# Performance work log

Measured on AMD Instinct MI355X. Metric: run time of the kernel, lower is better.

The kernel has to match this reference:

```python
import jax, jax.numpy as jnp
import numpy as np
from jax import lax

NUM_SUPERNODES = 1024
KNN_K = 16
MIN_GRIPPER = 16
MIN_MASK = 8
GRIP_START = 0
GRIP_RADIUS = 0.1
NEG_INF = -jnp.inf


def _take(a, idx):
    return jnp.take_along_axis(a, idx, axis=1)


def _scatter_or(idx, keep, Bf, N):
    # OR `keep` into a fresh [Bf,N] bool mask at positions idx (mirrors torch scatter_)
    b = jnp.arange(Bf)[:, None]
    return jnp.zeros((Bf, N), dtype=bool).at[b, idx].max(keep)


def _cdist(a, b):
    # a [B,M,3], b [B,N,3] -> [B,M,N] euclidean
    d2 = (jnp.sum(a * a, -1)[:, :, None] + jnp.sum(b * b, -1)[:, None, :]
          - 2.0 * jnp.einsum('bmd,bnd->bmn', a, b))
    return jnp.sqrt(jnp.maximum(d2, 0.0))


def _sample_supernodes(xyz, valid, state, mask_id, extra_scores, global_scores):
    Bf, N, _ = xyz.shape
    M = NUM_SUPERNODES
    valid = valid.astype(bool)
    row_has_valid = valid.any(axis=1)
    first_valid = jnp.argmax(valid, axis=1).astype(jnp.int32)  # [Bf]

    # ---- gripper quota: nearest points to gripper xyz (within radius if any) ----
    k_grip = min(MIN_GRIPPER, M)
    gxyz = state[:, GRIP_START:GRIP_START + 3]
    gdist = jnp.linalg.norm(xyz - gxyz[:, None, :], axis=-1)  # [Bf,N]
    in_radius = gdist <= GRIP_RADIUS
    has_radius = (valid & in_radius).any(axis=1, keepdims=True)
    eligible = valid & (in_radius | ~has_radius)
    dist_rank = jnp.where(eligible, gdist, jnp.inf)
    neg_vals, grip_idx = lax.top_k(-dist_rank, k_grip)
    grip_vals = -neg_vals
    grip_keep = jnp.isfinite(grip_vals) & row_has_valid[:, None]
    head_idx = jnp.where(grip_keep, grip_idx, first_valid[:, None])
    head_bucket = jnp.where(grip_keep, 1, -1)
    selected = _scatter_or(grip_idx, grip_keep, Bf, N)

    remaining = M - k_grip
    # ---- mask-instance quota: one point per mask id (dedup via sort) ----
    mask_cand = valid & ~selected
    sentinel = jnp.iinfo(mask_id.dtype).max
    mask_key = jnp.where(mask_cand, mask_id, sentinel)
    sort_idx = jnp.argsort(mask_key, axis=1)
    sorted_valid = _take(mask_cand, sort_idx)
    sorted_mask = _take(mask_id, sort_idx)
    first_for_id = jnp.concatenate(
        [sorted_valid[:, :1],
         sorted_valid[:, 1:] & (sorted_mask[:, 1:] != sorted_mask[:, :-1])], axis=1)
    pos = jnp.arange(N, dtype=jnp.float32)[None, :]
    mask_scores = jnp.where(first_for_id, -pos, NEG_INF)
    mask_vals, mask_pos = lax.top_k(mask_scores, remaining)
    mask_idx = _take(sort_idx, mask_pos)
    mask_keep = jnp.isfinite(mask_vals) & row_has_valid[:, None]
    selected_after_mask = selected | _scatter_or(mask_idx, mask_keep, Bf, N)

    # ---- extra random mask supernodes to guarantee min_mask quota ----
    k_extra = min(MIN_MASK, remaining)
    es = jnp.where(valid & ~selected_after_mask, extra_scores, NEG_INF)
    extra_vals, extra_idx = lax.top_k(es, k_extra)
    extra_keep = jnp.isfinite(extra_vals) & row_has_valid[:, None]
    use_extra = ~mask_keep[:, :k_extra] & extra_keep
    mask_idx = mask_idx.at[:, :k_extra].set(
        jnp.where(use_extra, extra_idx, mask_idx[:, :k_extra]))
    mask_keep = mask_keep.at[:, :k_extra].set(mask_keep[:, :k_extra] | use_extra)

    # ---- global random fill ----
    selected_for_global = selected | _scatter_or(mask_idx, mask_keep, Bf, N)
    gs = jnp.where(valid & ~selected_for_global, global_scores, NEG_INF)
    gvals, gidx = lax.top_k(gs, remaining)
    gkeep = jnp.isfinite(gvals) & row_has_valid[:, None]
    fill_idx = jnp.where(mask_keep, mask_idx,
                         jnp.where(gkeep, gidx, first_valid[:, None]))
    fill_bucket = jnp.where(mask_keep, 2, jnp.where(gkeep, 0, -1))

    out_idx = jnp.concatenate([head_idx, fill_idx], axis=1)
    out_bucket = jnp.concatenate([head_bucket, fill_bucket], axis=1)
    out_valid = _take(valid, out_idx) & row_has_valid[:, None]
    out_bucket = jnp.where(out_valid, out_bucket, -1)
    return out_idx, out_valid, out_bucket


def setup_inputs() -> dict:
    key = jax.random.key(0)
    ks = jax.random.split(key, 6)
    Bf, N, C = 8, 16384, 64
    return {
        'x': jax.random.normal(ks[0], (Bf, N, C), dtype=jnp.float32),
        'xyz': jax.random.normal(ks[1], (Bf, N, 3), dtype=jnp.float32),
        'valid': jnp.ones((Bf, N), dtype=bool),
        'state': jax.random.normal(ks[2], (Bf, 8), dtype=jnp.float32),
        'mask_id': jax.random.randint(ks[3], (Bf, N), 0, 32, dtype=jnp.int32),
        'extra_scores': jax.random.uniform(ks[4], (Bf, N), dtype=jnp.float32),
        'global_scores': jax.random.uniform(ks[5], (Bf, N), dtype=jnp.float32),
    }


def reference(x, xyz, valid, state, mask_id, extra_scores, global_scores):
    Bf, N, C = x.shape
    out_idx, out_valid, out_bucket = _sample_supernodes(
        xyz, valid, state, mask_id, extra_scores, global_scores)
    # gather_points
    supernode_xyz = _take(xyz, out_idx[:, :, None].repeat(3, axis=2))  # [Bf,M,3]
    # build_knn_neighbors: masked cdist + topk smallest
    dist = _cdist(supernode_xyz.astype(jnp.float32), xyz.astype(jnp.float32))
    dist = jnp.where(valid.astype(bool)[:, None, :], dist, jnp.inf)
    neg_vals, neighbor_idx = lax.top_k(-dist, KNN_K)
    neighbor_mask = jnp.isfinite(-neg_vals)  # [Bf,M,K]
    # gather_neighbors
    b = jnp.arange(Bf)[:, None, None]
    neighbor_feats = x[b, neighbor_idx]  # [Bf,M,K,C]
    return (neighbor_feats, supernode_xyz, neighbor_mask,
            out_idx, out_valid, out_bucket)
```

## Files before the change

### kernel.cpp

```cpp
#include <hip/hip_runtime.h>
#include <math.h>

typedef unsigned long long u64;
typedef unsigned int u32;

#define BF 8
#define NPTS 16384
#define HALFPTS 8192
#define M_SN 1024
#define CCH 64
#define KNN 16
#define NTHR1 1024
#define KPER 16
#define TBL 4096
#define CCAP 2048
#define REM 1008

constexpr size_t O0 = 0;
constexpr size_t O1 = 8388608;
constexpr size_t O2 = 8413184;
constexpr size_t O3 = 8544256;
constexpr size_t O4 = 8552448;
constexpr size_t O5 = 8560640;

#define PW_OFF ((size_t)256)
#define PW_BYTES ((size_t)BF * NPTS * 16)
#define WN_BYTES ((size_t)2 * BF * M_SN * KNN * 8)

__device__ __forceinline__ bool is_valid_el(const void* vp, int mode, long long i) {
  if (mode == 1) return ((const unsigned char*)vp)[i] != 0;
  if (mode == 2) return ((const float*)vp)[i] != 0.0f;
  return ((const int*)vp)[i] != 0;
}

__device__ __forceinline__ u32 desc_enc(float f) {
  u32 u = __float_as_uint(f);
  u32 s = (u & 0x80000000u) ? ~u : (u | 0x80000000u);
  return ~s;
}
__device__ __forceinline__ bool enc_finite(u32 d) {
  u32 s = ~d;
  u32 u = (s & 0x80000000u) ? (s & 0x7FFFFFFFu) : ~s;
  return (u & 0x7F800000u) != 0x7F800000u;
}

__device__ __forceinline__ u64 wave_min_u64(u64 v) {
#pragma unroll
  for (int d = 32; d >= 1; d >>= 1) {
    u32 lo = __shfl_xor((u32)(v & 0xFFFFFFFFu), d, 64);
    u32 hi = __shfl_xor((u32)(v >> 32), d, 64);
    u64 o = ((u64)hi << 32) | lo;
    if (o < v) v = o;
  }
  return v;
}

__device__ __forceinline__ u64 block_min_u64(u64 v, u64* red16, int t) {
  v = wave_min_u64(v);
  if ((t & 63) == 0) red16[t >> 6] = v;
  __syncthreads();
  if (t < 64) {
    u64 x = red16[t & 15];
    x = wave_min_u64(x);
    if (t == 0) red16[0] = x;
  }
  __syncthreads();
  u64 r = red16[0];
  __syncthreads();
  return r;
}

__device__ __forceinline__ int block_excl_scan(int val, int* scanb, int t, int* tot) {
  int incl = val;
#pragma unroll
  for (int d = 1; d < 64; d <<= 1) {
    int v = __shfl_up(incl, d, 64);
    if ((t & 63) >= d) incl += v;
  }
  if ((t & 63) == 63) scanb[t >> 6] = incl;
  __syncthreads();
  if (t < 64) {
    int ws = (t < 16) ? scanb[t] : 0;
#pragma unroll
    for (int d = 1; d < 16; d <<= 1) {
      int v = __shfl_up(ws, d, 64);
      if ((t & 63) >= d) ws += v;
    }
    if (t < 16) scanb[16 + t] = ws;
  }
  __syncthreads();
  int wv = t >> 6;
  int base = (wv == 0) ? 0 : scanb[16 + wv - 1];
  *tot = scanb[16 + 15];
  int r = base + incl - val;
  __syncthreads();
  return r;
}

__device__ __forceinline__ u64 shfl64_grp(u64 v, int src) {
  u32 lo = (u32)__shfl((int)(u32)(v & 0xFFFFFFFFu), src, 32);
  u32 hi = (u32)__shfl((int)(u32)(v >> 32), src, 32);
  return ((u64)hi << 32) | lo;
}

template<bool ASC, bool SHIFTBIN>
__device__ __forceinline__ void topk_select(const u32* ek, const u32* bk, u32 cmask,
    int Twant, int* table, u64* cand, int* scanb, int* sh, int* outArr, int t) {
  for (int j = t; j < TBL; j += NTHR1) table[j] = 0;
  if (t == 6) sh[6] = 0x7FFFFFFF;
  if (t == 7) sh[7] = 1;
  __syncthreads();
#pragma unroll
  for (int k = 0; k < KPER; k++) {
    if ((cmask >> k) & 1u) {
      int bin = SHIFTBIN ? (int)(ek[k] >> 20) : (int)bk[k];
      atomicAdd(&table[bin], 1);
    }
  }
  __syncthreads();
  int c_[4]; int c4 = 0;
#pragma unroll
  for (int q = 0; q < 4; q++) { c_[q] = table[4 * t + q]; c4 += c_[q]; }
  int htot;
  int cum = block_excl_scan(c4, scanb, t, &htot);
  const int T = min(Twant, htot);
  int e_ = cum;
#pragma unroll
  for (int q = 0; q < 4; q++) {
    int nx = e_ + c_[q];
    if (T > 0 && e_ < T && nx >= T) atomicMin(&sh[6], 4 * t + q);
    table[4 * t + q] = e_;
    e_ = nx;
  }
  __syncthreads();
  if (T <= 0) return;
  const int B = sh[6];
#pragma unroll
  for (int k = 0; k < KPER; k++) {
    if ((cmask >> k) & 1u) {
      int bin = SHIFTBIN ? (int)(ek[k] >> 20) : (int)bk[k];
      if (bin <= B) {
        int pos = atomicAdd(&table[bin], 1);
        if (pos < CCAP)
          cand[pos] = ((u64)ek[k] << 32) | ((u64)(u32)bin << 14) | (u32)(k * NTHR1 + t);
      }
    }
  }
  __syncthreads();
  const int nc = table[B];
  if (nc <= CCAP) {
    for (int c = t; c < nc; c += NTHR1) {
      u64 key = cand[c];
      int bin = (int)((key >> 14) & 0xFFFu);
      int s = bin ? table[bin - 1] : 0;
      int e2 = table[bin];
      int r = s;
      for (int j = s; j < e2; j++) r += (cand[j] < key);
      if (r < T) {
        u32 enc = (u32)(key >> 32);
        int ix = (int)(key & 0x3FFFu);
        bool fin = ASC ? (enc < 0x7F800000u) : enc_finite(enc);
        outArr[r] = fin ? ix : (ix | (int)0x80000000);
      }
    }
  } else {
    if (t == 0) sh[7] = 0;
  }
  __syncthreads();
}

__global__ void detect_valid(const unsigned* __restrict__ w, int nwords, int* __restrict__ flag) {
  __shared__ int cls;
  int t = threadIdx.x;
  if (t == 0) cls = 0;
  __syncthreads();
  int local = 0;
  for (int i = t; i < nwords; i += blockDim.x) {
    unsigned v = w[i];
    if (v == 0x3F800000u) local = 2;
    else if (v != 0u && v != 1u) local = max(local, 1);
  }
  if (local) atomicMax(&cls, local);
  __syncthreads();
  if (t == 0) flag[0] = cls;
}

__global__ __launch_bounds__(1024)
void sample_kernel(const float* __restrict__ xyz, const void* __restrict__ validp,
                   const float* __restrict__ state, const int* __restrict__ mask_id,
                   const float* __restrict__ extra, const float* __restrict__ glob,
                   const int* __restrict__ flagp, float4* __restrict__ pw,
                   float* __restrict__ out) {
  __shared__ u64 red16[16];
  __shared__ int table[TBL];
  __shared__ int scanb[32];
  __shared__ int mpick[REM];
  __shared__ u64 cand[CCAP];
  __shared__ int gsorted[REM];
  __shared__ int head_i[16];
  __shared__ int head_bk[16];
  __shared__ int sh[8];

  const int b = blockIdx.x, t = threadIdx.x;
  const int vmode = flagp[0];
  const float* xyzb = xyz + (size_t)b * NPTS * 3;
  const int* midb = mask_id + (size_t)b * NPTS;
  const float* exb = extra + (size_t)b * NPTS;
  const float* glb = glob + (size_t)b * NPTS;

  if (t < 8) sh[t] = 0;
  if (t == 1) sh[1] = 0x7FFFFFFF;
  if (t < 16) gsorted[t] = -1;
  __syncthreads();

  u32 vbits = 0;
#pragma unroll
  for (int k = 0; k < KPER; k++) {
    int i = k * NTHR1 + t;
    if (is_valid_el(validp, vmode, (long long)b * NPTS + i)) vbits |= 1u << k;
  }
  if (vbits) {
    atomicOr(&sh[0], 1);
    atomicMin(&sh[1], (__ffs(vbits) - 1) * NTHR1 + t);
  }

  float gx = state[b * 8 + 0], gy = state[b * 8 + 1], gz = state[b * 8 + 2];
  float gd[KPER];
  u32 inr = 0;
#pragma unroll
  for (int k = 0; k < KPER; k++) {
    int i = k * NTHR1 + t;
    float px = xyzb[3 * i], py = xyzb[3 * i + 1], pz = xyzb[3 * i + 2];
    float dx = px - gx, dy = py - gy, dz = pz - gz;
    float d = sqrtf((dx * dx + dy * dy) + dz * dz);
    gd[k] = d;
    bool vb = (vbits >> k) & 1u;
    if (vb && d <= 0.1f) inr |= 1u << k;
    if (pw) {
      float sb = __fadd_rn(__fadd_rn(__fmul_rn(px, px), __fmul_rn(py, py)), __fmul_rn(pz, pz));
      pw[(size_t)b * NPTS + i] = make_float4(px, py, pz, vb ? sb : INFINITY);
    }
  }
  if (inr) atomicOr(&sh[2], 1);
  __syncthreads();

  const int rhv = sh[0];
  const int first_valid = rhv ? sh[1] : 0;
  const u32 elig = vbits & (sh[2] ? inr : 0xFFFFu);
  u32 sel = 0;

  {
    u32 ek[KPER];
#pragma unroll
    for (int k = 0; k < KPER; k++) ek[k] = __float_as_uint(gd[k]);
    topk_select<true, true>(ek, nullptr, elig, 16, table, cand, scanb, sh, gsorted, t);
    if (sh[7]) {
      if (t < 16) {
        int g = gsorted[t];
        head_i[t] = (g >= 0) ? g : first_valid;
        head_bk[t] = (g >= 0) ? 1 : -1;
      }
      __syncthreads();
      for (int j = 0; j < 16; j++) {
        if (head_bk[j] == 1) {
          int ix = head_i[j];
          if ((ix & (NTHR1 - 1)) == t) sel |= 1u << (ix >> 10);
        }
      }
    } else {
      for (int it = 0; it < 16; ++it) {
        u64 best = ~0ull;
#pragma unroll
        for (int k = 0; k < KPER; k++) {
          if (((elig >> k) & 1u) && !((sel >> k) & 1u)) {
            u64 key = ((u64)__float_as_uint(gd[k]) << 32) | (u32)(k * NTHR1 + t);
            if (key < best) best = key;
          }
        }
        u64 w = block_min_u64(best, red16, t);
        bool keep = (w >> 32) < 0x7F800000ull;
        int idx = (int)(w & 0xFFFFFFFFu);
        if (t == 0) { head_i[it] = keep ? idx : first_valid; head_bk[it] = keep ? 1 : -1; }
        if (keep && (idx & (NTHR1 - 1)) == t) sel |= 1u << (idx >> 10);
      }
      __syncthreads();
    }
  }

  for (int j = t; j < TBL; j += NTHR1) table[j] = 0x7FFFFFFF;
  __syncthreads();
#pragma unroll
  for (int k = 0; k < KPER; k++) {
    if (((vbits >> k) & 1u) && !((sel >> k) & 1u)) {
      int i = k * NTHR1 + t;
      int id = midb[i];
      if ((u32)id < TBL) atomicMin(&table[id], i);
    }
  }
  __syncthreads();
  int cnt = 0;
#pragma unroll
  for (int q = 0; q < 4; q++) cnt += (table[4 * t + q] != 0x7FFFFFFF);
  int mtot;
  int excl = block_excl_scan(cnt, scanb, t, &mtot);
  {
    int pos = excl;
#pragma unroll
    for (int q = 0; q < 4; q++) {
      int v = table[4 * t + q];
      if (v != 0x7FFFFFFF) { if (pos < REM) mpick[pos] = v; pos++; }
    }
  }
  __syncthreads();
  const int nm = min(mtot, REM);
  for (int j = 0; j < nm; j++) {
    int p = mpick[j];
    if ((p & (NTHR1 - 1)) == t) sel |= 1u << (p >> 10);
  }

  u32 extra_used = 0;
  if (nm < 8 && rhv) {
    u32 extrbits = 0;
    for (int j = 0; j < 8; j++) {
      u64 best = ~0ull;
#pragma unroll
      for (int k = 0; k < KPER; k++) {
        if (((vbits >> k) & 1u) && !((sel >> k) & 1u) && !((extrbits >> k) & 1u)) {
          int i = k * NTHR1 + t;
          u64 key = ((u64)desc_enc(exb[i]) << 32) | (u32)i;
          if (key < best) best = key;
        }
      }
      u64 w = block_min_u64(best, red16, t);
      if (w == ~0ull) break;
      int idx = (int)(w & 0xFFFFFFFFu);
      bool fin = enc_finite((u32)(w >> 32));
      if ((idx & (NTHR1 - 1)) == t) extrbits |= 1u << (idx >> 10);
      if (j >= nm && fin) {
        extra_used |= 1u << j;
        if (t == 0) mpick[j] = idx;
        if ((idx & (NTHR1 - 1)) == t) sel |= 1u << (idx >> 10);
      }
    }
    __syncthreads();
  }

  {
    u32 cbits = vbits & ~sel;
    u32 ek[KPER], bk[KPER];
#pragma unroll
    for (int k = 0; k < KPER; k++) {
      if ((cbits >> k) & 1u) {
        float f = glb[k * NTHR1 + t];
        ek[k] = desc_enc(f);
        float g = fminf(fmaxf(f, 0.0f), 0.99999994f);
        bk[k] = 4095u - (u32)(g * 4096.0f);
      } else { ek[k] = 0xFFFFFFFFu; bk[k] = 4095u; }
    }
    for (int j = t; j < REM; j += NTHR1) gsorted[j] = -1;
    topk_select<false, false>(ek, bk, cbits, REM, table, cand, scanb, sh, gsorted, t);
    if (!sh[7]) {
      u32 gext = 0;
      for (int j = 0; j < REM; j++) {
        u64 best = ~0ull;
#pragma unroll
        for (int k = 0; k < KPER; k++) {
          if (((cbits >> k) & 1u) && !((gext >> k) & 1u)) {
            u64 key = ((u64)ek[k] << 32) | (u32)(k * NTHR1 + t);
            if (key < best) best = key;
          }
        }
        u64 w = block_min_u64(best, red16, t);
        if (w == ~0ull) break;
        int idx = (int)(w & 0xFFFFFFFFu);
        if ((idx & (NTHR1 - 1)) == t) gext |= 1u << (idx >> 10);
        if (t == 0) gsorted[j] = enc_finite((u32)(w >> 32)) ? idx : (idx | (int)0x80000000);
      }
      __syncthreads();
    }
  }

  {
    int slot = t;
    int idx, bucket;
    if (slot < 16) {
      idx = head_i[slot];
      bucket = head_bk[slot];
    } else {
      int jj = slot - 16;
      bool mk = (jj < nm) || (jj < 8 && ((extra_used >> jj) & 1u));
      if (mk) { idx = mpick[jj]; bucket = 2; }
      else {
        int g = gsorted[jj];
        if (rhv && g >= 0) { idx = g; bucket = 0; }
        else { idx = first_valid; bucket = -1; }
      }
    }
    bool ov = rhv && is_valid_el(validp, vmode, (long long)b * NPTS + idx);
    int ob = ov ? bucket : -1;
    size_t o = (size_t)b * M_SN + slot;
    out[O3 + o] = (float)idx;
    out[O4 + o] = ov ? 1.0f : 0.0f;
    out[O5 + o] = (float)ob;
    out[O1 + 3 * o + 0] = xyzb[3 * idx + 0];
    out[O1 + 3 * o + 1] = xyzb[3 * idx + 1];
    out[O1 + 3 * o + 2] = xyzb[3 * idx + 2];
  }
}

#define NTHR2 256
#define CH 1024
#define SPB 8
#define GCAP 64

__global__ __launch_bounds__(256, 4)
void knn_kernel(const float* __restrict__ x, const float* __restrict__ xyz,
                const void* __restrict__ validp, const int* __restrict__ flagp,
                const float4* __restrict__ pw, u64* __restrict__ wnws,
                float* __restrict__ out) {
  __shared__ __align__(16) float4 st[CH];
  __shared__ float bqf[(NTHR2 / 32) * GCAP];
  __shared__ int bqi[(NTHR2 / 32) * GCAP];
  __shared__ u64 wn[SPB * KNN];

  const int b = blockIdx.x >> 7;
  const int grp = blockIdx.x & 127;
  const int half = blockIdx.y;
  const int t = threadIdx.x;
  const int g = t >> 5;
  const int sub = t & 31;
  const int lanebase = t & 32;
  const int m = grp * SPB + g;
  const float* xyzb = xyz + (size_t)b * NPTS * 3;

  const int sidx = (int)out[O3 + (size_t)b * M_SN + m];
  float ax, ay, az;
  if (pw) { float4 qv = pw[(size_t)b * NPTS + sidx]; ax = qv.x; ay = qv.y; az = qv.z; }
  else { ax = xyzb[3 * sidx]; ay = xyzb[3 * sidx + 1]; az = xyzb[3 * sidx + 2]; }
  const float a2x = ax + ax, a2y = ay + ay, a2z = az + az;

  float ld = -INFINITY;
  int li = 0;
  float kq = -INFINITY;
  int bn = 0;
  float* gbq = bqf + g * GCAP;
  int* gbi = bqi + g * GCAP;

  const int vmode = pw ? 0 : flagp[0];
  const int cbeg = wnws ? half * HALFPTS : 0;
  const int cend = wnws ? cbeg + HALFPTS : NPTS;

  for (int c0 = cbeg; c0 < cend; c0 += CH) {
    if (pw) {
      const float4* src = pw + (size_t)b * NPTS + c0;
#pragma unroll
      for (int qq = 0; qq < CH / NTHR2; qq++) st[t + qq * NTHR2] = src[t + qq * NTHR2];
    } else {
      for (int p = t; p < CH; p += NTHR2) {
        float px = xyzb[3 * (c0 + p)], py = xyzb[3 * (c0 + p) + 1], pz = xyzb[3 * (c0 + p) + 2];
        bool v = is_valid_el(validp, vmode, (long long)b * NPTS + c0 + p);
        float sb = __fadd_rn(__fadd_rn(__fmul_rn(px, px), __fmul_rn(py, py)), __fmul_rn(pz, pz));
        st[p] = make_float4(px, py, pz, v ? sb : INFINITY);
      }
    }
    __syncthreads();

    int jstart = 0;
    if (c0 == cbeg) {
      float4 v = st[sub];
      float qv = __builtin_fmaf(a2x, v.x, __builtin_fmaf(a2y, v.y, __builtin_fmaf(a2z, v.z, -v.w)));
      int qi = c0 + sub;
#pragma unroll
      for (int p = 0; p < 32; p++) {
        int par;
        if ((p & 1) == 0) par = sub ^ 1;
        else par = (sub == 0 || sub == 31) ? sub : (((sub - 1) ^ 1) + 1);
        float oq = __shfl(qv, par, 32);
        int oi = __shfl(qi, par, 32);
        if (par != sub) {
          bool lo = sub < par;
          bool take = lo ? (oq > qv) : (oq < qv);
          if (take) { qv = oq; qi = oi; }
        }
      }
      ld = qv; li = qi;
      kq = __shfl(ld, 15, 32);
      jstart = 1;
    }

#pragma unroll 4
    for (int j = jstart; j < CH / 32; j++) {
      float4 v = st[sub + 32 * j];
      float qv = __builtin_fmaf(a2x, v.x, __builtin_fmaf(a2y, v.y, __builtin_fmaf(a2z, v.z, -v.w)));
      u64 bal = __ballot(qv > kq);
      u32 mqg = (u32)(bal >> lanebase);
      if (mqg) {
        if (qv > kq) {
          int pos = bn + __popc(mqg & ((1u << sub) - 1u));
          if (pos < GCAP) { gbq[pos] = qv; gbi[pos] = c0 + 32 * j + sub; }
        }
        bn += __popc(mqg);
      }
    }

    if (bn > GCAP) {
      for (int j = jstart; j < CH / 32; j++) {
        float4 v = st[sub + 32 * j];
        float qv = __builtin_fmaf(a2x, v.x, __builtin_fmaf(a2y, v.y, __builtin_fmaf(a2z, v.z, -v.w)));
        u64 bal = __ballot(qv > kq);
        u32 mq = (u32)(bal >> lanebase);
        while (mq) {
          int bb = __ffs(mq) - 1;
          mq &= mq - 1;
          float kd = __shfl(qv, lanebase + bb, 64);
          if (kd > kq) {
            int ki = c0 + 32 * j + bb;
            bool gt = ld < kd;
            float sd = __shfl_up(ld, 1, 32);
            int si = __shfl_up(li, 1, 32);
            int pg = __shfl_up(gt ? 1 : 0, 1, 32);
            if (sub == 0) pg = 0;
            ld = gt ? (pg ? sd : kd) : ld;
            li = gt ? (pg ? si : ki) : li;
            kq = __shfl(ld, 15, 32);
          }
        }
      }
    } else {
      for (int c = 0; c < bn; c++) {
        float kd = gbq[c];
        int ki = gbi[c];
        if (kd > kq) {
          bool gt = ld < kd;
          float sd = __shfl_up(ld, 1, 32);
          int si = __shfl_up(li, 1, 32);
          int pg = __shfl_up(gt ? 1 : 0, 1, 32);
          if (sub == 0) pg = 0;
          ld = gt ? (pg ? sd : kd) : ld;
          li = gt ? (pg ? si : ki) : li;
          kq = __shfl(ld, 15, 32);
        }
      }
    }
    bn = 0;
    __syncthreads();
  }

  if (wnws) {
    if (sub < KNN)
      wnws[((size_t)half * BF + b) * M_SN * KNN + (size_t)m * KNN + sub] =
          ((u64)desc_enc(ld) << 32) | (u32)li;
    return;
  }

  if (sub < KNN) wn[g * KNN + sub] = ((u64)desc_enc(ld) << 32) | (u32)li;
  __syncthreads();
  {
    int s2 = t >> 5;
    int k2 = (t >> 1) & 15;
    int hf = t & 1;
    int mm = grp * SPB + s2;
    u64 key = wn[s2 * KNN + k2];
    int ni = (int)(key & (u64)(NPTS - 1));
    size_t o2 = ((size_t)b * M_SN + mm) * KNN + k2;
    if (hf == 0) out[O2 + o2] = enc_finite((u32)(key >> 32)) ? 1.0f : 0.0f;
    const float4* src = (const float4*)(x + ((size_t)b * NPTS + ni) * CCH);
    float4* dst = (float4*)(out + O0 + o2 * CCH);
#pragma unroll
    for (int q = 0; q < 8; q++) dst[hf * 8 + q] = src[hf * 8 + q];
  }
}

__global__ __launch_bounds__(256)
void knn_merge_kernel(const float* __restrict__ x, const u64* __restrict__ wnws,
                      float* __restrict__ out) {
  __shared__ u64 wn[SPB * KNN];
  const int b = blockIdx.x >> 7;
  const int grp = blockIdx.x & 127;
  const int t = threadIdx.x;
  const int sl = t >> 5;
  const int sub = t & 31;
  const int m = grp * SPB + sl;

  const int h = sub >> 4, k = sub & 15;
  u64 my = wnws[((size_t)h * BF + b) * M_SN * KNN + (size_t)m * KNN + k];
  const int obase = (1 - h) << 4;
  int cnt2 = 0;
#pragma unroll
  for (int j = 0; j < 16; j++) {
    u64 o = shfl64_grp(my, obase + j);
    cnt2 += h ? (o <= my) : (o < my);
  }
  int rank = k + cnt2;
  if (rank < KNN) wn[sl * KNN + rank] = my;
  __syncthreads();

  {
    int s2 = t >> 5;
    int k2 = (t >> 1) & 15;
    int hf = t & 1;
    int mm = grp * SPB + s2;
    u64 key = wn[s2 * KNN + k2];
    int ni = (int)(key & (u64)(NPTS - 1));
    size_t o2 = ((size_t)b * M_SN + mm) * KNN + k2;
    if (hf == 0) out[O2 + o2] = enc_finite((u32)(key >> 32)) ? 1.0f : 0.0f;
    const float4* src = (const float4*)(x + ((size_t)b * NPTS + ni) * CCH);
    float4* dst = (float4*)(out + O0 + o2 * CCH);
#pragma unroll
    for (int q = 0; q < 8; q++) dst[hf * 8 + q] = src[hf * 8 + q];
  }
}

extern "C" void kernel_launch(void* const* d_in, const int* in_sizes, int n_in,
                              void* d_out, int out_size, void* d_ws, size_t ws_size,
                              hipStream_t stream) {
  const float* x = (const float*)d_in[0];
  const float* xyz = (const float*)d_in[1];
  const void* valid = d_in[2];
  const float* state = (const float*)d_in[3];
  const int* mask_id = (const int*)d_in[4];
  const float* extra = (const float*)d_in[5];
  const float* glob = (const float*)d_in[6];
  float* out = (float*)d_out;
  int* flag = (int*)d_ws;

  float4* pw = nullptr;
  u64* wnws = nullptr;
  if (ws_size >= PW_OFF + PW_BYTES) pw = (float4*)((char*)d_ws + PW_OFF);
  if (pw && ws_size >= PW_OFF + PW_BYTES + WN_BYTES)
    wnws = (u64*)((char*)d_ws + PW_OFF + PW_BYTES);

  detect_valid<<<1, 1024, 0, stream>>>((const unsigned*)valid, in_sizes[2] / 4, flag);
  sample_kernel<<<BF, NTHR1, 0, stream>>>(xyz, valid, state, mask_id, extra, glob, flag, pw, out);
  dim3 kg(BF * 128, wnws ? 2 : 1);
  knn_kernel<<<kg, NTHR2, 0, stream>>>(x, xyz, valid, flag, pw, wnws, out);
  if (wnws) knn_merge_kernel<<<BF * 128, NTHR2, 0, stream>>>(x, wnws, out);
}
```

Measured before the change: 289.6 us.

## Parallelize valid detection across blocks and simplify KNN candidate insertion

The valid-type detection kernel now runs on 64 blocks with wave-level shuffle reduction and a global atomicMax, after a memset of the flag, replacing the single-block scan. In the KNN kernel, the per-group shared candidate buffer and its two-pass overflow fallback are removed, and ballot hits are inserted directly into the register top-k list inside the scan loop. Dropping that shared memory allows higher occupancy, so launch bounds go from 4 to 8 blocks per CU. The risk is that inserting serially inside the hot loop may cost more than batched insertion once the candidate rate is high, and the extra memset adds a small launch.

```diff
diff --git a/kernel.cpp b/kernel.cpp
--- a/kernel.cpp
+++ b/kernel.cpp
@@ -170,19 +170,15 @@
 }
 
 __global__ void detect_valid(const unsigned* __restrict__ w, int nwords, int* __restrict__ flag) {
-  __shared__ int cls;
-  int t = threadIdx.x;
-  if (t == 0) cls = 0;
-  __syncthreads();
   int local = 0;
-  for (int i = t; i < nwords; i += blockDim.x) {
+  for (int i = blockIdx.x * blockDim.x + threadIdx.x; i < nwords; i += gridDim.x * blockDim.x) {
     unsigned v = w[i];
     if (v == 0x3F800000u) local = 2;
     else if (v != 0u && v != 1u) local = max(local, 1);
   }
-  if (local) atomicMax(&cls, local);
-  __syncthreads();
-  if (t == 0) flag[0] = cls;
+#pragma unroll
+  for (int d = 32; d >= 1; d >>= 1) local = max(local, __shfl_xor(local, d, 64));
+  if ((threadIdx.x & 63) == 0 && local) atomicMax(flag, local);
 }
 
 __global__ __launch_bounds__(1024)
@@ -411,40 +407,35 @@
 #define NTHR2 256
 #define CH 1024
 #define SPB 8
-#define GCAP 64
-
-__global__ __launch_bounds__(256, 4)
+
+__global__ __launch_bounds__(256, 8)
 void knn_kernel(const float* __restrict__ x, const float* __restrict__ xyz,
                 const void* __restrict__ validp, const int* __restrict__ flagp,
                 const float4* __restrict__ pw, u64* __restrict__ wnws,
                 float* __restrict__ out) {
   __shared__ __align__(16) float4 st[CH];
-  __shared__ float bqf[(NTHR2 / 32) * GCAP];
-  __shared__ int bqi[(NTHR2 / 32) * GCAP];
   __shared__ u64 wn[SPB * KNN];
 
   const int b = blockIdx.x >> 7;
   const int grp = blockIdx.x & 127;
   const int half = blockIdx.y;
   const int t = threadIdx.x;
-  const int g = t >> 5;
+  const int sl = t >> 5;
   const int sub = t & 31;
   const int lanebase = t & 32;
-  const int m = grp * SPB + g;
+  const int m = grp * SPB + sl;
   const float* xyzb = xyz + (size_t)b * NPTS * 3;
+  const long long gbase = (long long)b * NPTS;
 
   const int sidx = (int)out[O3 + (size_t)b * M_SN + m];
   float ax, ay, az;
-  if (pw) { float4 qv = pw[(size_t)b * NPTS + sidx]; ax = qv.x; ay = qv.y; az = qv.z; }
+  if (pw) { float4 c = pw[gbase + sidx]; ax = c.x; ay = c.y; az = c.z; }
   else { ax = xyzb[3 * sidx]; ay = xyzb[3 * sidx + 1]; az = xyzb[3 * sidx + 2]; }
   const float a2x = ax + ax, a2y = ay + ay, a2z = az + az;
 
   float ld = -INFINITY;
   int li = 0;
   float kq = -INFINITY;
-  int bn = 0;
-  float* gbq = bqf + g * GCAP;
-  int* gbi = bqi + g * GCAP;
 
   const int vmode = pw ? 0 : flagp[0];
   const int cbeg = wnws ? half * HALFPTS : 0;
@@ -452,13 +443,13 @@
 
   for (int c0 = cbeg; c0 < cend; c0 += CH) {
     if (pw) {
-      const float4* src = pw + (size_t)b * NPTS + c0;
+      const float4* src = pw + gbase + c0;
 #pragma unroll
       for (int qq = 0; qq < CH / NTHR2; qq++) st[t + qq * NTHR2] = src[t + qq * NTHR2];
     } else {
       for (int p = t; p < CH; p += NTHR2) {
         float px = xyzb[3 * (c0 + p)], py = xyzb[3 * (c0 + p) + 1], pz = xyzb[3 * (c0 + p) + 2];
-        bool v = is_valid_el(validp, vmode, (long long)b * NPTS + c0 + p);
+        bool v = is_valid_el(validp, vmode, gbase + c0 + p);
         float sb = __fadd_rn(__fadd_rn(__fmul_rn(px, px), __fmul_rn(py, py)), __fmul_rn(pz, pz));
         st[p] = make_float4(px, py, pz, v ? sb : INFINITY);
       }
@@ -493,44 +484,13 @@
       float4 v = st[sub + 32 * j];
       float qv = __builtin_fmaf(a2x, v.x, __builtin_fmaf(a2y, v.y, __builtin_fmaf(a2z, v.z, -v.w)));
       u64 bal = __ballot(qv > kq);
-      u32 mqg = (u32)(bal >> lanebase);
-      if (mqg) {
-        if (qv > kq) {
-          int pos = bn + __popc(mqg & ((1u << sub) - 1u));
-          if (pos < GCAP) { gbq[pos] = qv; gbi[pos] = c0 + 32 * j + sub; }
-        }
-        bn += __popc(mqg);
-      }
-    }
-
-    if (bn > GCAP) {
-      for (int j = jstart; j < CH / 32; j++) {
-        float4 v = st[sub + 32 * j];
-        float qv = __builtin_fmaf(a2x, v.x, __builtin_fmaf(a2y, v.y, __builtin_fmaf(a2z, v.z, -v.w)));
-        u64 bal = __ballot(qv > kq);
-        u32 mq = (u32)(bal >> lanebase);
-        while (mq) {
-          int bb = __ffs(mq) - 1;
-          mq &= mq - 1;
-          float kd = __shfl(qv, lanebase + bb, 64);
-          if (kd > kq) {
-            int ki = c0 + 32 * j + bb;
-            bool gt = ld < kd;
-            float sd = __shfl_up(ld, 1, 32);
-            int si = __shfl_up(li, 1, 32);
-            int pg = __shfl_up(gt ? 1 : 0, 1, 32);
-            if (sub == 0) pg = 0;
-            ld = gt ? (pg ? sd : kd) : ld;
-            li = gt ? (pg ? si : ki) : li;
-            kq = __shfl(ld, 15, 32);
-          }
-        }
-      }
-    } else {
-      for (int c = 0; c < bn; c++) {
-        float kd = gbq[c];
-        int ki = gbi[c];
+      u32 mq = (u32)(bal >> lanebase);
+      while (mq) {
+        int bb = __ffs(mq) - 1;
+        mq &= mq - 1;
+        float kd = __shfl(qv, lanebase + bb, 64);
         if (kd > kq) {
+          int ki = c0 + 32 * j + bb;
           bool gt = ld < kd;
           float sd = __shfl_up(ld, 1, 32);
           int si = __shfl_up(li, 1, 32);
@@ -542,7 +502,6 @@
         }
       }
     }
-    bn = 0;
     __syncthreads();
   }
 
@@ -553,7 +512,7 @@
     return;
   }
 
-  if (sub < KNN) wn[g * KNN + sub] = ((u64)desc_enc(ld) << 32) | (u32)li;
+  if (sub < KNN) wn[sl * KNN + sub] = ((u64)desc_enc(ld) << 32) | (u32)li;
   __syncthreads();
   {
     int s2 = t >> 5;
@@ -564,7 +523,7 @@
     int ni = (int)(key & (u64)(NPTS - 1));
     size_t o2 = ((size_t)b * M_SN + mm) * KNN + k2;
     if (hf == 0) out[O2 + o2] = enc_finite((u32)(key >> 32)) ? 1.0f : 0.0f;
-    const float4* src = (const float4*)(x + ((size_t)b * NPTS + ni) * CCH);
+    const float4* src = (const float4*)(x + (gbase + ni) * CCH);
     float4* dst = (float4*)(out + O0 + o2 * CCH);
 #pragma unroll
     for (int q = 0; q < 8; q++) dst[hf * 8 + q] = src[hf * 8 + q];
@@ -630,7 +589,8 @@
   if (pw && ws_size >= PW_OFF + PW_BYTES + WN_BYTES)
     wnws = (u64*)((char*)d_ws + PW_OFF + PW_BYTES);
 
-  detect_valid<<<1, 1024, 0, stream>>>((const unsigned*)valid, in_sizes[2] / 4, flag);
+  hipMemsetAsync(flag, 0, 4, stream);
+  detect_valid<<<64, 1024, 0, stream>>>((const unsigned*)valid, in_sizes[2] / 4, flag);
   sample_kernel<<<BF, NTHR1, 0, stream>>>(xyz, valid, state, mask_id, extra, glob, flag, pw, out);
   dim3 kg(BF * 128, wnws ? 2 : 1);
   knn_kernel<<<kg, NTHR2, 0, stream>>>(x, xyz, valid, flag, pw, wnws, out);
```

After: 264.9 us. 8.5% less time.
